# Kernel optimization log

Hardware: AMD Instinct MI355X
Metric: run time of the kernel (lower is better)

Reference implementation:

```python
import jax, jax.numpy as jnp
import numpy as np

H = 512  # hidden_dim

def setup_inputs() -> dict:
    key = jax.random.key(0)
    k1, k2, k3, k4, k5 = jax.random.split(key, 5)
    B, S = 32, 2048
    hidden = jax.random.normal(k1, (B, 2 * H), dtype=jnp.float32)
    encoder_outputs = jax.random.normal(k2, (B, S, 2 * H), dtype=jnp.float32)
    # nn.Linear(4H, H): weight [H, 4H], bias [H]
    W = jax.random.normal(k3, (H, 4 * H), dtype=jnp.float32) / np.sqrt(4 * H)
    b = jnp.zeros((H,), dtype=jnp.float32)
    v = jax.random.normal(k4, (H,), dtype=jnp.float32) / np.sqrt(H)
    return {"hidden": hidden, "encoder_outputs": encoder_outputs, "W": W, "b": b, "v": v}

def reference(hidden, encoder_outputs, W, b, v):
    B, S, _ = encoder_outputs.shape
    # concat repeated decoder hidden with encoder outputs: [B, S, 4H]
    hidden_rep = jnp.broadcast_to(hidden[:, None, :], (B, S, hidden.shape[-1]))
    cat = jnp.concatenate([hidden_rep, encoder_outputs], axis=-1)
    energy = jnp.tanh(jnp.einsum('bsf,hf->bsh', cat, W) + b)  # [B, S, H]
    scores = jnp.einsum('bsh,h->bs', energy, v)               # [B, S]
    attn = jax.nn.softmax(scores, axis=1)                     # softmax over seq
    context = jnp.einsum('bsd,bs->bd', encoder_outputs, attn) # [B, 2H]
    return context
```

## Files before the change

### kernel.cpp

```cpp
#include <hip/hip_runtime.h>


typedef __fp16   half2v __attribute__((ext_vector_type(2)));
typedef _Float16 half8  __attribute__((ext_vector_type(8)));
typedef __attribute__((ext_vector_type(4)))  float f4;
typedef __attribute__((ext_vector_type(16))) float f16v;
typedef __attribute__((ext_vector_type(4)))  unsigned int uint4v;

__device__ __forceinline__ void gload_lds16(const void* g, void* l) {
    __builtin_amdgcn_global_load_lds(
        (const __attribute__((address_space(1))) unsigned int*)g,
        (__attribute__((address_space(3))) unsigned int*)l, 16, 0, 0);
}
__device__ __forceinline__ unsigned int bc2(half2v h) {
    return __builtin_bit_cast(unsigned int, h);
}

__global__ __launch_bounds__(256) void prep_kernel(
    const float* __restrict__ hidden, const float* __restrict__ W,
    const float* __restrict__ bias, float* __restrict__ u,
    unsigned short* __restrict__ w2) {
    if (blockIdx.x < 64) {
        int t = blockIdx.x * 256 + threadIdx.x;
        int b = t >> 9, h = t & 511;
        const f4* wr = (const f4*)(W + (size_t)h * 2048);
        const f4* hr = (const f4*)(hidden + (size_t)b * 1024);
        float acc = bias[h];
        #pragma unroll 4
        for (int i = 0; i < 256; ++i) {
            f4 w4 = wr[i]; f4 h4 = hr[i];
            acc += w4[0]*h4[0] + w4[1]*h4[1] + w4[2]*h4[2] + w4[3]*h4[3];
        }
        u[t] = acc;
    } else {
        int g = (blockIdx.x - 64) * 256 + threadIdx.x;
        int kk = g >> 11, id = g & 2047;
        int ntg = id >> 7, kh = (id >> 6) & 1, l = id & 63;
        int h = (ntg << 5) + (l & 31);
        int kg = 1024 + (kk << 5) + (kh << 4) + ((l >> 5) << 3);
        const float* src = W + (size_t)h * 2048 + kg;
        f4 x0 = *(const f4*)src;
        f4 x1 = *(const f4*)(src + 4);
        half8 vh;
        #pragma unroll
        for (int j = 0; j < 4; ++j) vh[j] = (_Float16)x0[j];
        #pragma unroll
        for (int j = 0; j < 4; ++j) vh[4 + j] = (_Float16)x1[j];
        ((half8*)w2)[g] = vh;
    }
}

__global__ __launch_bounds__(256, 3) void score_kernel(
    const float* __restrict__ enc, const unsigned short* __restrict__ w2,
    const float* __restrict__ u, const float* __restrict__ v,
    float* __restrict__ scores_part) {
    __shared__ short Ahi[2048], Alo[2048];
    __shared__ short Bs[8192];
    __shared__ float u_s[256], v_s[256];
    __shared__ float partial[4][64];

    const int tid  = threadIdx.x;
    const int wl   = tid >> 6, lane = tid & 63;
    const int col  = lane & 31;
    const int sblk = blockIdx.x >> 1, hh = blockIdx.x & 1;
    const int row0 = sblk * 64;
    const int b    = row0 >> 11;
    const float* encB = enc + (size_t)row0 * 1024;

    u_s[tid] = u[(b << 9) + (hh << 8) + tid];
    v_s[tid] = v[(hh << 8) + tid];

    f16v acc[2][2];
    #pragma unroll
    for (int mt = 0; mt < 2; ++mt)
        #pragma unroll
        for (int nt = 0; nt < 2; ++nt)
            #pragma unroll
            for (int r = 0; r < 16; ++r) acc[mt][nt][r] = 0.f;

    const int s_mt = tid >> 7, s_kh = (tid >> 6) & 1, s_l = tid & 63;
    const int s_row = (s_mt << 5) + (s_l & 31);
    const int s_kb  = (s_kh << 4) + ((s_l >> 5) << 3);
    const float* aSrc = encB + (size_t)s_row * 1024 + s_kb;

    const half8* Ah8 = (const half8*)Ahi;
    const half8* Al8 = (const half8*)Alo;
    const half8* Bh8 = (const half8*)Bs;

    for (int kk = 0; kk < 32; ++kk) {
        f4 x0 = *(const f4*)(aSrc + (kk << 5));
        f4 x1 = *(const f4*)(aSrc + (kk << 5) + 4);
        __syncthreads();
        {
            half2v h01 = __builtin_amdgcn_cvt_pkrtz(x0[0], x0[1]);
            half2v h23 = __builtin_amdgcn_cvt_pkrtz(x0[2], x0[3]);
            half2v h45 = __builtin_amdgcn_cvt_pkrtz(x1[0], x1[1]);
            half2v h67 = __builtin_amdgcn_cvt_pkrtz(x1[2], x1[3]);
            half2v l01 = __builtin_amdgcn_cvt_pkrtz(x0[0] - (float)h01[0], x0[1] - (float)h01[1]);
            half2v l23 = __builtin_amdgcn_cvt_pkrtz(x0[2] - (float)h23[0], x0[3] - (float)h23[1]);
            half2v l45 = __builtin_amdgcn_cvt_pkrtz(x1[0] - (float)h45[0], x1[1] - (float)h45[1]);
            half2v l67 = __builtin_amdgcn_cvt_pkrtz(x1[2] - (float)h67[0], x1[3] - (float)h67[1]);
            uint4v hp = {bc2(h01), bc2(h23), bc2(h45), bc2(h67)};
            uint4v lp = {bc2(l01), bc2(l23), bc2(l45), bc2(l67)};
            ((uint4v*)Ahi)[tid] = hp;
            ((uint4v*)Alo)[tid] = lp;
        }
        {
            const char* bsrc = (const char*)w2 + (size_t)kk * 32768 + (hh << 14)
                               + (wl << 12) + lane * 16;
            char* bdst = (char*)Bs + (wl << 12);
            #pragma unroll
            for (int i = 0; i < 4; ++i)
                gload_lds16(bsrc + (i << 10), bdst + (i << 10));
        }
        __syncthreads();
        #pragma unroll
        for (int kh = 0; kh < 2; ++kh) {
            half8 ah0 = Ah8[(kh << 6) + lane];
            half8 ah1 = Ah8[128 + (kh << 6) + lane];
            half8 al0 = Al8[(kh << 6) + lane];
            half8 al1 = Al8[128 + (kh << 6) + lane];
            #pragma unroll
            for (int nt = 0; nt < 2; ++nt) {
                int ntl = (wl << 1) + nt;
                half8 b8 = Bh8[((ntl << 1) + kh) * 64 + lane];
                acc[0][nt] = __builtin_amdgcn_mfma_f32_32x32x16_f16(ah0, b8, acc[0][nt], 0, 0, 0);
                acc[0][nt] = __builtin_amdgcn_mfma_f32_32x32x16_f16(al0, b8, acc[0][nt], 0, 0, 0);
                acc[1][nt] = __builtin_amdgcn_mfma_f32_32x32x16_f16(ah1, b8, acc[1][nt], 0, 0, 0);
                acc[1][nt] = __builtin_amdgcn_mfma_f32_32x32x16_f16(al1, b8, acc[1][nt], 0, 0, 0);
            }
        }
    }
    const int rhalf = (lane >> 5) << 2;
    #pragma unroll
    for (int mt = 0; mt < 2; ++mt) {
        #pragma unroll
        for (int reg = 0; reg < 16; ++reg) {
            float ssum = 0.f;
            #pragma unroll
            for (int nt = 0; nt < 2; ++nt) {
                int hl = (((wl << 1) + nt) << 5) + col;
                float x = u_s[hl] + acc[mt][nt][reg];
                float t = __expf(2.f * x);
                float th = 1.f - 2.f / (t + 1.f);
                ssum += v_s[hl] * th;
            }
            ssum += __shfl_xor(ssum, 1);
            ssum += __shfl_xor(ssum, 2);
            ssum += __shfl_xor(ssum, 4);
            ssum += __shfl_xor(ssum, 8);
            ssum += __shfl_xor(ssum, 16);
            if (col == 0)
                partial[wl][(mt << 5) + (reg & 3) + ((reg >> 2) << 3) + rhalf] = ssum;
        }
    }
    __syncthreads();
    if (tid < 64) {
        float s = partial[0][tid] + partial[1][tid] + partial[2][tid] + partial[3][tid];
        scores_part[(hh << 16) + row0 + tid] = s;
    }
}

__global__ __launch_bounds__(256) void ctx_partial_kernel(
    const float* __restrict__ enc, const float* __restrict__ scores_part,
    float* __restrict__ partials) {
    __shared__ float p_s[2048];
    __shared__ float wredm[4], wreds[4];
    const int t = threadIdx.x;
    const int b = blockIdx.x >> 5, sc = blockIdx.x & 31;
    const int wid = t >> 6, lane = t & 63;
    const float* s0 = scores_part + ((size_t)b << 11);
    const float* s1 = s0 + 65536;

    float vals[8];
    float mx = -1e30f;
    #pragma unroll
    for (int i = 0; i < 8; ++i) {
        int idx = t + (i << 8);
        vals[i] = s0[idx] + s1[idx];
        mx = fmaxf(mx, vals[i]);
    }
    #pragma unroll
    for (int off = 1; off < 64; off <<= 1) mx = fmaxf(mx, __shfl_xor(mx, off));
    if (lane == 0) wredm[wid] = mx;
    __syncthreads();
    mx = fmaxf(fmaxf(wredm[0], wredm[1]), fmaxf(wredm[2], wredm[3]));

    float lsum = 0.f;
    #pragma unroll
    for (int i = 0; i < 8; ++i) {
        float e = __expf(vals[i] - mx);
        p_s[t + (i << 8)] = e;
        lsum += e;
    }
    #pragma unroll
    for (int off = 1; off < 64; off <<= 1) lsum += __shfl_xor(lsum, off);
    if (lane == 0) wreds[wid] = lsum;
    __syncthreads();
    const float inv = 1.f / (wreds[0] + wreds[1] + wreds[2] + wreds[3]);

    f4 a = (f4){0.f, 0.f, 0.f, 0.f};
    const f4* erow = ((const f4*)(enc + ((size_t)b * 2048 + (sc << 6)) * 1024)) + t;
    #pragma unroll 4
    for (int i = 0; i < 64; ++i) {
        float p = p_s[(sc << 6) + i] * inv;
        f4 e = erow[(size_t)i << 8];
        a += p * e;
    }
    f4* dst = (f4*)(partials + (((size_t)(sc << 5) + b) << 10));
    dst[t] = a;
}

__global__ __launch_bounds__(256) void ctx_reduce_kernel(
    const float* __restrict__ partials, float* __restrict__ out) {
    int i = blockIdx.x * 256 + threadIdx.x;
    float s = 0.f;
    #pragma unroll
    for (int sc = 0; sc < 32; ++sc) s += partials[sc * 32768 + i];
    out[i] = s;
}

extern "C" void kernel_launch(void* const* d_in, const int* in_sizes, int n_in,
                              void* d_out, int out_size, void* d_ws, size_t ws_size,
                              hipStream_t stream) {
    const float* hidden = (const float*)d_in[0];
    const float* enc    = (const float*)d_in[1];
    const float* W      = (const float*)d_in[2];
    const float* bias   = (const float*)d_in[3];
    const float* v      = (const float*)d_in[4];
    float* out = (float*)d_out;
    char* ws = (char*)d_ws;

    float* u            = (float*)(ws);
    float* scores_part  = (float*)(ws + 65536);
    float* partials     = (float*)(ws + 589824);
    unsigned short* w2  = (unsigned short*)(ws + 4784128);

    prep_kernel<<<320, 256, 0, stream>>>(hidden, W, bias, u, w2);
    score_kernel<<<2048, 256, 0, stream>>>(enc, w2, u, v, scores_part);
    ctx_partial_kernel<<<1024, 256, 0, stream>>>(enc, scores_part, partials);
    ctx_reduce_kernel<<<128, 256, 0, stream>>>(partials, out);
}
```

Measured before the change: 548.7 us.

## Double-buffer LDS tiles and prefetch encoder rows two steps ahead

Splits the A (hi/lo fp16) and B shared-memory tiles into two buffers so that staging of the next K-slice overlaps the MFMA work on the current slice. Encoder global loads are issued two iterations ahead into registers, and one barrier per iteration replaces two. This hides global and LDS load latency but doubles LDS usage and adds register pressure, which could lower occupancy.

```diff
diff --git a/kernel.cpp b/kernel.cpp
--- a/kernel.cpp
+++ b/kernel.cpp
@@ -54,8 +54,8 @@
     const float* __restrict__ enc, const unsigned short* __restrict__ w2,
     const float* __restrict__ u, const float* __restrict__ v,
     float* __restrict__ scores_part) {
-    __shared__ short Ahi[2048], Alo[2048];
-    __shared__ short Bs[8192];
+    __shared__ short Ahi[2][2048], Alo[2][2048];
+    __shared__ short Bs[2][8192];
     __shared__ float u_s[256], v_s[256];
     __shared__ float partial[4][64];
 
@@ -83,37 +83,49 @@
     const int s_kb  = (s_kh << 4) + ((s_l >> 5) << 3);
     const float* aSrc = encB + (size_t)s_row * 1024 + s_kb;
 
-    const half8* Ah8 = (const half8*)Ahi;
-    const half8* Al8 = (const half8*)Alo;
-    const half8* Bh8 = (const half8*)Bs;
-
+    auto stageA = [&](int buf, const f4& x0, const f4& x1) {
+        half2v h01 = __builtin_amdgcn_cvt_pkrtz(x0[0], x0[1]);
+        half2v h23 = __builtin_amdgcn_cvt_pkrtz(x0[2], x0[3]);
+        half2v h45 = __builtin_amdgcn_cvt_pkrtz(x1[0], x1[1]);
+        half2v h67 = __builtin_amdgcn_cvt_pkrtz(x1[2], x1[3]);
+        half2v l01 = __builtin_amdgcn_cvt_pkrtz(x0[0] - (float)h01[0], x0[1] - (float)h01[1]);
+        half2v l23 = __builtin_amdgcn_cvt_pkrtz(x0[2] - (float)h23[0], x0[3] - (float)h23[1]);
+        half2v l45 = __builtin_amdgcn_cvt_pkrtz(x1[0] - (float)h45[0], x1[1] - (float)h45[1]);
+        half2v l67 = __builtin_amdgcn_cvt_pkrtz(x1[2] - (float)h67[0], x1[3] - (float)h67[1]);
+        uint4v hp = {bc2(h01), bc2(h23), bc2(h45), bc2(h67)};
+        uint4v lp = {bc2(l01), bc2(l23), bc2(l45), bc2(l67)};
+        ((uint4v*)Ahi[buf])[tid] = hp;
+        ((uint4v*)Alo[buf])[tid] = lp;
+    };
+    auto stageB = [&](int buf, int kk) {
+        const char* bsrc = (const char*)w2 + (size_t)kk * 32768 + (hh << 14)
+                           + (wl << 12) + lane * 16;
+        char* bdst = (char*)Bs[buf] + (wl << 12);
+        #pragma unroll
+        for (int i = 0; i < 4; ++i)
+            gload_lds16(bsrc + (i << 10), bdst + (i << 10));
+    };
+
+    f4 pf0[2], pf1[2];
+    pf0[0] = *(const f4*)(aSrc);           pf1[0] = *(const f4*)(aSrc + 4);
+    pf0[1] = *(const f4*)(aSrc + 32);      pf1[1] = *(const f4*)(aSrc + 36);
+    stageA(0, pf0[0], pf1[0]);
+    stageB(0, 0);
+    __syncthreads();
+
+    #pragma unroll 2
     for (int kk = 0; kk < 32; ++kk) {
-        f4 x0 = *(const f4*)(aSrc + (kk << 5));
-        f4 x1 = *(const f4*)(aSrc + (kk << 5) + 4);
-        __syncthreads();
-        {
-            half2v h01 = __builtin_amdgcn_cvt_pkrtz(x0[0], x0[1]);
-            half2v h23 = __builtin_amdgcn_cvt_pkrtz(x0[2], x0[3]);
-            half2v h45 = __builtin_amdgcn_cvt_pkrtz(x1[0], x1[1]);
-            half2v h67 = __builtin_amdgcn_cvt_pkrtz(x1[2], x1[3]);
-            half2v l01 = __builtin_amdgcn_cvt_pkrtz(x0[0] - (float)h01[0], x0[1] - (float)h01[1]);
-            half2v l23 = __builtin_amdgcn_cvt_pkrtz(x0[2] - (float)h23[0], x0[3] - (float)h23[1]);
-            half2v l45 = __builtin_amdgcn_cvt_pkrtz(x1[0] - (float)h45[0], x1[1] - (float)h45[1]);
-            half2v l67 = __builtin_amdgcn_cvt_pkrtz(x1[2] - (float)h67[0], x1[3] - (float)h67[1]);
-            uint4v hp = {bc2(h01), bc2(h23), bc2(h45), bc2(h67)};
-            uint4v lp = {bc2(l01), bc2(l23), bc2(l45), bc2(l67)};
-            ((uint4v*)Ahi)[tid] = hp;
-            ((uint4v*)Alo)[tid] = lp;
-        }
-        {
-            const char* bsrc = (const char*)w2 + (size_t)kk * 32768 + (hh << 14)
-                               + (wl << 12) + lane * 16;
-            char* bdst = (char*)Bs + (wl << 12);
-            #pragma unroll
-            for (int i = 0; i < 4; ++i)
-                gload_lds16(bsrc + (i << 10), bdst + (i << 10));
-        }
-        __syncthreads();
+        const int cur = kk & 1, nxt = cur ^ 1;
+        const int k2 = (kk + 2 <= 31) ? kk + 2 : 31;
+        f4 t0 = *(const f4*)(aSrc + (k2 << 5));
+        f4 t1 = *(const f4*)(aSrc + (k2 << 5) + 4);
+        if (kk < 31) {
+            stageA(nxt, pf0[nxt], pf1[nxt]);
+            stageB(nxt, kk + 1);
+        }
+        const half8* Ah8 = (const half8*)Ahi[cur];
+        const half8* Al8 = (const half8*)Alo[cur];
+        const half8* Bh8 = (const half8*)Bs[cur];
         #pragma unroll
         for (int kh = 0; kh < 2; ++kh) {
             half8 ah0 = Ah8[(kh << 6) + lane];
@@ -130,6 +142,8 @@
                 acc[1][nt] = __builtin_amdgcn_mfma_f32_32x32x16_f16(al1, b8, acc[1][nt], 0, 0, 0);
             }
         }
+        pf0[cur] = t0; pf1[cur] = t1;
+        __syncthreads();
     }
     const int rhalf = (lane >> 5) << 2;
     #pragma unroll
```

Result: no change. 555.1 us (+1.2%).
